# Kernel tuning notes

Measured on AMD Instinct MI355X. Metric: run time of the kernel, lower is better.

The kernel has to match this reference:

```python
import jax, jax.numpy as jnp
import numpy as np

NUM_EMBEDDINGS = 8192
EMBEDDING_DIM = 256
BETA = 0.25


def setup_inputs() -> dict:
    key = jax.random.key(0)
    k1, k2 = jax.random.split(key)
    z = jax.random.normal(k1, (16, 256, 32, 32), dtype=jnp.float32)
    # nn.Embedding weight init: uniform(-1/K, 1/K)
    emb = jax.random.uniform(k2, (NUM_EMBEDDINGS, EMBEDDING_DIM), dtype=jnp.float32,
                             minval=-1.0 / NUM_EMBEDDINGS, maxval=1.0 / NUM_EMBEDDINGS)
    return {"z": z, "emb": emb}


def reference(z, emb):
    b, c, h, w = z.shape
    flat = z.transpose(0, 2, 3, 1).reshape(-1, c)  # [B*H*W, C]
    distances = (jnp.sum(flat * flat, axis=1, keepdims=True)
                 - 2.0 * flat @ emb.T
                 + jnp.sum(emb * emb, axis=1))  # [B*H*W, K]
    indices = jnp.argmin(distances, axis=1)  # [B*H*W]
    quantized = emb[indices].reshape(b, h, w, c).transpose(0, 3, 1, 2)  # [B,C,H,W]
    codebook_loss = jnp.mean((jax.lax.stop_gradient(quantized) - z) ** 2)
    commitment_loss = BETA * jnp.mean((quantized - jax.lax.stop_gradient(z)) ** 2)
    quantized_st = z + jax.lax.stop_gradient(quantized - z)  # straight-through
    return quantized_st, codebook_loss, commitment_loss, indices.reshape(b, h, w)
```

## Files before the change

### kernel.cpp

```cpp
#include <hip/hip_runtime.h>

#define NROWS   16384
#define KCODES  8192
#define CDIM    256
#define HWS     1024
#define BSTRIDE 262144

#define WS_AN   0
#define WS_CE   16384
#define WS_CD   24576
#define WS_CI   155648
#define WS_IDX  286720
#define WS_LOSS 303104

__global__ void rownorm_z_k(const float* __restrict__ z, float* __restrict__ An) {
#pragma clang fp contract(off)
  int n = blockIdx.x * 256 + threadIdx.x;
  const float* base = z + ((size_t)(n >> 10)) * BSTRIDE + (n & 1023);
  float hs[2];
  for (int h = 0; h < 2; ++h) {
    float r[8];
#pragma unroll
    for (int j = 0; j < 8; ++j) { float v = base[(size_t)(h * 128 + j) * HWS]; r[j] = v * v; }
    for (int m = 1; m < 16; ++m) {
#pragma unroll
      for (int j = 0; j < 8; ++j) { float v = base[(size_t)(h * 128 + m * 8 + j) * HWS]; r[j] += v * v; }
    }
    hs[h] = ((r[0] + r[1]) + (r[2] + r[3])) + ((r[4] + r[5]) + (r[6] + r[7]));
  }
  An[n] = hs[0] + hs[1];
}

__global__ void rownorm_e_k(const float* __restrict__ emb, float* __restrict__ Ce) {
#pragma clang fp contract(off)
  int n = blockIdx.x * 256 + threadIdx.x;
  const float* base = emb + (size_t)n * CDIM;
  float hs[2];
  for (int h = 0; h < 2; ++h) {
    float r[8];
#pragma unroll
    for (int j = 0; j < 8; ++j) { float v = base[h * 128 + j]; r[j] = v * v; }
    for (int m = 1; m < 16; ++m) {
#pragma unroll
      for (int j = 0; j < 8; ++j) { float v = base[h * 128 + m * 8 + j]; r[j] += v * v; }
    }
    hs[h] = ((r[0] + r[1]) + (r[2] + r[3])) + ((r[4] + r[5]) + (r[6] + r[7]));
  }
  Ce[n] = hs[0] + hs[1];
}

__global__ void __launch_bounds__(256)
vq_argmin_k(const float* __restrict__ z, const float* __restrict__ emb,
            const float* __restrict__ An, const float* __restrict__ Ce,
            float* __restrict__ cand_d, int* __restrict__ cand_i) {
  __shared__ float smem[8192];
  float* As = smem;
  float* Bs = smem + 4096;

  const int t  = threadIdx.x;
  const int tx = t & 15;
  const int ty = t >> 4;
  const int tile  = blockIdx.x >> 3;
  const int slice = blockIdx.x & 7;
  const int rbase = tile * 128;
  const int k0    = slice * 1024;

  const float* zb = z + ((size_t)(rbase >> 10)) * BSTRIDE + (rbase & 1023);

  float best[8];
  int   bidx[8];
#pragma unroll
  for (int ri = 0; ri < 8; ++ri) { best[ri] = 3.4028235e38f; bidx[ri] = 0; }

  float acc[8][8];
#pragma unroll
  for (int ri = 0; ri < 8; ++ri)
#pragma unroll
    for (int ci = 0; ci < 8; ++ci) acc[ri][ci] = 0.f;

  const int a_c   = t >> 4;
  const int a_hw  = (t & 15) * 8;
  const int a_swr = (t & 15) & 7;
  const int a_wi  = a_c & 3;
  const int a_kg1 = a_c >> 2;
  const int acol1 = ((a_kg1 ^ a_swr) << 2) | a_wi;
  const int acol2 = (((a_kg1 + 4) ^ a_swr) << 2) | a_wi;
  const int b_code  = t >> 1;
  const int b_cb    = (t & 1) * 16;
  const int b_swr   = (t >> 1) & 7;
  const int b_kg0   = b_cb >> 2;

  const int rd_a_sw = ty & 7;
  const int rd_b_sw = tx & 7;

  for (int kc = 0; kc < 8; ++kc) {
    const int kbase = k0 + kc * 128;
#pragma unroll 1
    for (int sc = 0; sc < 8; ++sc) {
      const float* zsrc = zb + (size_t)(sc * 32 + a_c) * HWS + a_hw;
      const float4 pa0 = *(const float4*)(zsrc);
      const float4 pa1 = *(const float4*)(zsrc + 4);
      const float4 pa2 = *(const float4*)(zsrc + 16 * HWS);
      const float4 pa3 = *(const float4*)(zsrc + 16 * HWS + 4);
      const float* bsrc = emb + (size_t)(kbase + b_code) * CDIM + sc * 32 + b_cb;
      const float4 pb0 = *(const float4*)(bsrc);
      const float4 pb1 = *(const float4*)(bsrc + 4);
      const float4 pb2 = *(const float4*)(bsrc + 8);
      const float4 pb3 = *(const float4*)(bsrc + 12);

      __syncthreads();
      {
        const float va0[8] = {pa0.x, pa0.y, pa0.z, pa0.w, pa1.x, pa1.y, pa1.z, pa1.w};
        const float va1[8] = {pa2.x, pa2.y, pa2.z, pa2.w, pa3.x, pa3.y, pa3.z, pa3.w};
#pragma unroll
        for (int j = 0; j < 8; ++j) {
          const int rb = (a_hw + j) << 5;
          As[rb + acol1] = va0[j];
          As[rb + acol2] = va1[j];
        }
        const int bb = b_code << 5;
        *(float4*)&Bs[bb + (((b_kg0 + 0) ^ b_swr) << 2)] = pb0;
        *(float4*)&Bs[bb + (((b_kg0 + 1) ^ b_swr) << 2)] = pb1;
        *(float4*)&Bs[bb + (((b_kg0 + 2) ^ b_swr) << 2)] = pb2;
        *(float4*)&Bs[bb + (((b_kg0 + 3) ^ b_swr) << 2)] = pb3;
      }
      __syncthreads();

#pragma unroll
      for (int g = 0; g < 8; ++g) {
        float4 bf[8];
#pragma unroll
        for (int ci = 0; ci < 8; ++ci)
          bf[ci] = *(const float4*)&Bs[((tx + ci * 16) << 5) + ((g ^ rd_b_sw) << 2)];
#pragma unroll
        for (int ri = 0; ri < 8; ++ri) {
          const float4 a = *(const float4*)&As[((ty * 8 + ri) << 5) + ((g ^ rd_a_sw) << 2)];
#pragma unroll
          for (int ci = 0; ci < 8; ++ci) {
            acc[ri][ci] = fmaf(a.x, bf[ci].x, fmaf(a.y, bf[ci].y,
                          fmaf(a.z, bf[ci].z, fmaf(a.w, bf[ci].w, acc[ri][ci]))));
          }
        }
      }
    }

    {
      const int kkb = kbase + tx;
      float cearr[8];
#pragma unroll
      for (int ci = 0; ci < 8; ++ci) cearr[ci] = Ce[kkb + ci * 16];
#pragma unroll
      for (int ri = 0; ri < 8; ++ri) {
        const float Ar = An[rbase + ty * 8 + ri];
#pragma unroll
        for (int ci = 0; ci < 8; ++ci) {
          const float d = (Ar - 2.0f * acc[ri][ci]) + cearr[ci];
          if (d < best[ri]) { best[ri] = d; bidx[ri] = kkb + ci * 16; }
          acc[ri][ci] = 0.f;
        }
      }
    }
  }

  __syncthreads();
  float* redd = smem;
  int*   redi = (int*)(smem + 2048);
#pragma unroll
  for (int ri = 0; ri < 8; ++ri) {
    redd[(ty * 8 + ri) * 16 + tx] = best[ri];
    redi[(ty * 8 + ri) * 16 + tx] = bidx[ri];
  }
  __syncthreads();
  if (t < 128) {
    float bd = redd[t * 16];
    int   bi = redi[t * 16];
    for (int j = 1; j < 16; ++j) {
      const float d  = redd[t * 16 + j];
      const int   i2 = redi[t * 16 + j];
      if (d < bd || (d == bd && i2 < bi)) { bd = d; bi = i2; }
    }
    const int n = rbase + t;
    cand_d[n * 8 + slice] = bd;
    cand_i[n * 8 + slice] = bi;
  }
}

__global__ void vq_merge_k(const float* __restrict__ cand_d, const int* __restrict__ cand_i,
                           int* __restrict__ idx_final, float* __restrict__ idxf_out) {
  const int n = blockIdx.x * 256 + threadIdx.x;
  float bd = cand_d[n * 8];
  int   bi = cand_i[n * 8];
#pragma unroll
  for (int s = 1; s < 8; ++s) {
    const float d  = cand_d[n * 8 + s];
    const int   i2 = cand_i[n * 8 + s];
    if (d < bd || (d == bd && i2 < bi)) { bd = d; bi = i2; }
  }
  idx_final[n] = bi;
  idxf_out[n] = (float)bi;
}

__launch_bounds__(256)
__global__ void vq_gather_loss_k(const float* __restrict__ z, const float* __restrict__ emb,
                                 const int* __restrict__ idx_final,
                                 float* __restrict__ qout, float* __restrict__ loss_acc) {
  __shared__ float Qs[32 * 260];
  __shared__ int   kidx[32];
  __shared__ float warp_s[4];
  const int t = threadIdx.x;
  const int rbase = blockIdx.x * 32;
  if (t < 32) kidx[t] = idx_final[rbase + t];
  __syncthreads();
  {
    const int r = t >> 3, cp = t & 7;
    const float4* er = (const float4*)(emb + (size_t)kidx[r] * CDIM);
#pragma unroll
    for (int j = 0; j < 8; ++j) {
      const int c4 = cp + j * 8;
      const float4 v = er[c4];
      *(float4*)&Qs[r * 260 + c4 * 4] = v;
    }
  }
  __syncthreads();
  const int b = rbase >> 10, hw0 = rbase & 1023;
  const float* zb = z + (size_t)b * BSTRIDE + hw0;
  float* qb = qout + (size_t)b * BSTRIDE + hw0;
  float s = 0.f;
  const int hwl = t & 31, cg = t >> 5;
  for (int i = 0; i < 32; ++i) {
    const int c = cg * 32 + i;
    const float q  = Qs[hwl * 260 + c];
    const size_t off = (size_t)c * HWS + hwl;
    const float zv = zb[off];
    const float d  = q - zv;
    qb[off] = zv + d;
    s += d * d;
  }
  for (int off = 32; off; off >>= 1) s += __shfl_down(s, off, 64);
  if ((t & 63) == 0) warp_s[t >> 6] = s;
  __syncthreads();
  if (t == 0) atomicAdd(loss_acc, warp_s[0] + warp_s[1] + warp_s[2] + warp_s[3]);
}

__global__ void vq_finalize_k(const float* __restrict__ loss_acc, float* __restrict__ out_loss) {
  const float m = loss_acc[0] * (1.0f / 4194304.0f);
  out_loss[0] = m;
  out_loss[1] = 0.25f * m;
}

extern "C" void kernel_launch(void* const* d_in, const int* in_sizes, int n_in,
                              void* d_out, int out_size, void* d_ws, size_t ws_size,
                              hipStream_t stream) {
  (void)in_sizes; (void)n_in; (void)out_size; (void)ws_size;
  const float* z   = (const float*)d_in[0];
  const float* emb = (const float*)d_in[1];
  float* out      = (float*)d_out;
  float* q_out    = out;
  float* loss_out = out + 4194304;
  float* idxf_out = out + 4194306;

  float* ws       = (float*)d_ws;
  float* An       = ws + WS_AN;
  float* Ce       = ws + WS_CE;
  float* cand_d   = ws + WS_CD;
  int*   cand_i   = (int*)(ws + WS_CI);
  int*   idx_fin  = (int*)(ws + WS_IDX);
  float* loss_acc = ws + WS_LOSS;

  hipMemsetAsync(loss_acc, 0, sizeof(float), stream);
  rownorm_z_k<<<64, 256, 0, stream>>>(z, An);
  rownorm_e_k<<<32, 256, 0, stream>>>(emb, Ce);
  vq_argmin_k<<<1024, 256, 0, stream>>>(z, emb, An, Ce, cand_d, cand_i);
  vq_merge_k<<<64, 256, 0, stream>>>(cand_d, cand_i, idx_fin, idxf_out);
  vq_gather_loss_k<<<512, 256, 0, stream>>>(z, emb, idx_fin, q_out, loss_acc);
  vq_finalize_k<<<1, 1, 0, stream>>>(loss_acc, loss_out);
}
```

Measured before the change: 968.1 us.

## Use packed v_pk_fma_f32 with interleaved codebook shared-memory layout

Replaces scalar FMAs in the distance GEMM with inline-asm v_pk_fma_f32, so each instruction updates two codes' accumulators for one row. The codebook tile in shared memory is rearranged so that codes ci and ci+16 sit interleaved, letting one vector load feed packed pairs directly. The aim is to roughly halve FMA instruction issue. Inline asm may limit compiler scheduling, the scattered scalar LDS stores may add bank conflicts, and the changed summation order may alter ties in argmin.

Result: slower. 990.8 us (+2.3%).

```diff
diff --git a/kernel.cpp b/kernel.cpp
--- a/kernel.cpp
+++ b/kernel.cpp
@@ -12,6 +12,16 @@
 #define WS_CI   155648
 #define WS_IDX  286720
 #define WS_LOSS 303104
+
+typedef float f32x2 __attribute__((ext_vector_type(2)));
+typedef float f32x4 __attribute__((ext_vector_type(4)));
+
+#define PKFMA_LO(acc, a, b) \
+  asm("v_pk_fma_f32 %0, %1, %2, %0 op_sel:[0,0,0] op_sel_hi:[0,1,1]" \
+      : "+v"(acc) : "v"(a), "v"(b))
+#define PKFMA_HI(acc, a, b) \
+  asm("v_pk_fma_f32 %0, %1, %2, %0 op_sel:[1,0,0] op_sel_hi:[1,1,1]" \
+      : "+v"(acc) : "v"(a), "v"(b))
 
 __global__ void rownorm_z_k(const float* __restrict__ z, float* __restrict__ An) {
 #pragma clang fp contract(off)
@@ -72,11 +82,11 @@
 #pragma unroll
   for (int ri = 0; ri < 8; ++ri) { best[ri] = 3.4028235e38f; bidx[ri] = 0; }
 
-  float acc[8][8];
+  f32x2 acc2[8][4];
 #pragma unroll
   for (int ri = 0; ri < 8; ++ri)
 #pragma unroll
-    for (int ci = 0; ci < 8; ++ci) acc[ri][ci] = 0.f;
+    for (int j = 0; j < 4; ++j) acc2[ri][j] = (f32x2){0.f, 0.f};
 
   const int a_c   = t >> 4;
   const int a_hw  = (t & 15) * 8;
@@ -85,13 +95,16 @@
   const int a_kg1 = a_c >> 2;
   const int acol1 = ((a_kg1 ^ a_swr) << 2) | a_wi;
   const int acol2 = (((a_kg1 + 4) ^ a_swr) << 2) | a_wi;
-  const int b_code  = t >> 1;
-  const int b_cb    = (t & 1) * 16;
-  const int b_swr   = (t >> 1) & 7;
-  const int b_kg0   = b_cb >> 2;
+  const int b_code = t >> 1;
+  const int b_cb   = (t & 1) * 16;
+  const int b_p    = ((b_code >> 5) << 4) | (b_code & 15);
+  const int b_s    = (b_code >> 4) & 1;
+  const int b_p7   = b_code & 7;
+  const int b_base = b_p * 64 + ((b_cb >> 1) << 2) + b_s;
 
   const int rd_a_sw = ty & 7;
   const int rd_b_sw = tx & 7;
+  const int bB      = tx * 64;
 
   for (int kc = 0; kc < 8; ++kc) {
     const int kbase = k0 + kc * 128;
@@ -118,27 +131,44 @@
           As[rb + acol1] = va0[j];
           As[rb + acol2] = va1[j];
         }
-        const int bb = b_code << 5;
-        *(float4*)&Bs[bb + (((b_kg0 + 0) ^ b_swr) << 2)] = pb0;
-        *(float4*)&Bs[bb + (((b_kg0 + 1) ^ b_swr) << 2)] = pb1;
-        *(float4*)&Bs[bb + (((b_kg0 + 2) ^ b_swr) << 2)] = pb2;
-        *(float4*)&Bs[bb + (((b_kg0 + 3) ^ b_swr) << 2)] = pb3;
+        const float bval[16] = {pb0.x, pb0.y, pb0.z, pb0.w,
+                                pb1.x, pb1.y, pb1.z, pb1.w,
+                                pb2.x, pb2.y, pb2.z, pb2.w,
+                                pb3.x, pb3.y, pb3.z, pb3.w};
+#pragma unroll
+        for (int i = 0; i < 8; ++i) {
+          const int off = b_base + ((i ^ b_p7) << 2);
+          Bs[off]     = bval[2 * i];
+          Bs[off + 2] = bval[2 * i + 1];
+        }
       }
       __syncthreads();
 
 #pragma unroll
       for (int g = 0; g < 8; ++g) {
-        float4 bf[8];
-#pragma unroll
-        for (int ci = 0; ci < 8; ++ci)
-          bf[ci] = *(const float4*)&Bs[((tx + ci * 16) << 5) + ((g ^ rd_b_sw) << 2)];
+        const int sw0 = ((2 * g) ^ rd_b_sw) << 2;
+        const int sw1 = sw0 ^ 4;
+        f32x4 bv[8];
+#pragma unroll
+        for (int ci2 = 0; ci2 < 4; ++ci2) {
+          bv[ci2 * 2 + 0] = *(const f32x4*)&Bs[bB + ci2 * 1024 + sw0];
+          bv[ci2 * 2 + 1] = *(const f32x4*)&Bs[bB + ci2 * 1024 + sw1];
+        }
 #pragma unroll
         for (int ri = 0; ri < 8; ++ri) {
-          const float4 a = *(const float4*)&As[((ty * 8 + ri) << 5) + ((g ^ rd_a_sw) << 2)];
-#pragma unroll
-          for (int ci = 0; ci < 8; ++ci) {
-            acc[ri][ci] = fmaf(a.x, bf[ci].x, fmaf(a.y, bf[ci].y,
-                          fmaf(a.z, bf[ci].z, fmaf(a.w, bf[ci].w, acc[ri][ci]))));
+          const f32x4 a = *(const f32x4*)&As[((ty * 8 + ri) << 5) + ((g ^ rd_a_sw) << 2)];
+          const f32x2 a01 = __builtin_shufflevector(a, a, 0, 1);
+          const f32x2 a23 = __builtin_shufflevector(a, a, 2, 3);
+#pragma unroll
+          for (int ci2 = 0; ci2 < 4; ++ci2) {
+            const f32x2 bk0 = __builtin_shufflevector(bv[ci2 * 2 + 0], bv[ci2 * 2 + 0], 0, 1);
+            const f32x2 bk1 = __builtin_shufflevector(bv[ci2 * 2 + 0], bv[ci2 * 2 + 0], 2, 3);
+            const f32x2 bk2 = __builtin_shufflevector(bv[ci2 * 2 + 1], bv[ci2 * 2 + 1], 0, 1);
+            const f32x2 bk3 = __builtin_shufflevector(bv[ci2 * 2 + 1], bv[ci2 * 2 + 1], 2, 3);
+            PKFMA_HI(acc2[ri][ci2], a23, bk3);
+            PKFMA_LO(acc2[ri][ci2], a23, bk2);
+            PKFMA_HI(acc2[ri][ci2], a01, bk1);
+            PKFMA_LO(acc2[ri][ci2], a01, bk0);
           }
         }
       }
@@ -153,10 +183,12 @@
       for (int ri = 0; ri < 8; ++ri) {
         const float Ar = An[rbase + ty * 8 + ri];
 #pragma unroll
-        for (int ci = 0; ci < 8; ++ci) {
-          const float d = (Ar - 2.0f * acc[ri][ci]) + cearr[ci];
-          if (d < best[ri]) { best[ri] = d; bidx[ri] = kkb + ci * 16; }
-          acc[ri][ci] = 0.f;
+        for (int ci2 = 0; ci2 < 4; ++ci2) {
+          const float d0 = (Ar - 2.0f * acc2[ri][ci2].x) + cearr[2 * ci2];
+          if (d0 < best[ri]) { best[ri] = d0; bidx[ri] = kkb + ci2 * 32; }
+          const float d1 = (Ar - 2.0f * acc2[ri][ci2].y) + cearr[2 * ci2 + 1];
+          if (d1 < best[ri]) { best[ri] = d1; bidx[ri] = kkb + ci2 * 32 + 16; }
+          acc2[ri][ci2] = (f32x2){0.f, 0.f};
         }
       }
     }
```
